# Kernel tuning notes

Measured on AMD Instinct MI355X. Metric: run time of the kernel, lower is better.

Reference implementation:

```python
import jax, jax.numpy as jnp
import numpy as np

EMBED = 1024

def setup_inputs() -> dict:
    key = jax.random.key(0)
    ks = jax.random.split(key, 7)
    s = 1.0 / np.sqrt(EMBED)  # ~ torch Linear default init scale
    x = jax.random.normal(ks[0], (4, 2048, EMBED), dtype=jnp.float32)
    Wq = jax.random.uniform(ks[1], (EMBED, EMBED), jnp.float32, -s, s)
    bq = jax.random.uniform(ks[2], (EMBED,), jnp.float32, -s, s)
    Wk = jax.random.uniform(ks[3], (EMBED, EMBED), jnp.float32, -s, s)
    bk = jax.random.uniform(ks[4], (EMBED,), jnp.float32, -s, s)
    Wv = jax.random.uniform(ks[5], (EMBED, EMBED), jnp.float32, -s, s)
    bv = jax.random.uniform(ks[6], (EMBED,), jnp.float32, -s, s)
    return {"x": x, "Wq": Wq, "bq": bq, "Wk": Wk, "bk": bk, "Wv": Wv, "bv": bv}

def reference(x, Wq, bq, Wk, bk, Wv, bv):
    # torch nn.Linear: y = x @ W.T + b
    q = jnp.einsum('bse,oe->bso', x, Wq) + bq
    k = jnp.einsum('bse,oe->bso', x, Wk) + bk
    v = jnp.einsum('bse,oe->bso', x, Wv) + bv
    scale = 1.0 / jnp.sqrt(jnp.float32(x.shape[-1]))
    scores = jnp.einsum('bqd,bkd->bqk', q, k) * scale  # [B,S,S]
    weights = jax.nn.softmax(scores, axis=-1)
    return jnp.einsum('bqk,bkd->bqd', weights, v)
```

## Files before the change

### kernel.cpp

```cpp
#include <hip/hip_runtime.h>
#include <stdint.h>

#define B_   4
#define S_   2048
#define E_   1024
#define MQKV (B_ * S_)
#define LDP  2112

typedef __bf16 bf16x8 __attribute__((ext_vector_type(8)));
typedef float f32x4 __attribute__((ext_vector_type(4)));
typedef unsigned short u16;
typedef unsigned int u32;

__device__ __forceinline__ u16 f2bf(float x) {
  union { float f; u32 u; } c; c.f = x;
  u32 r = (c.u + 0x7FFFu + ((c.u >> 16) & 1u)) >> 16;
  return (u16)r;
}
__device__ __forceinline__ float bf2f(u16 h) {
  union { u32 u; float f; } c; c.u = ((u32)h) << 16;
  return c.f;
}

__global__ __launch_bounds__(256) void cvt_f32_bf16(const float* __restrict__ src,
                                                    u16* __restrict__ dst, int n4) {
  int i = blockIdx.x * blockDim.x + threadIdx.x;
  int st = gridDim.x * blockDim.x;
  for (; i < n4; i += st) {
    float4 f = reinterpret_cast<const float4*>(src)[i];
    ushort4 o;
    o.x = f2bf(f.x); o.y = f2bf(f.y); o.z = f2bf(f.z); o.w = f2bf(f.w);
    reinterpret_cast<ushort4*>(dst)[i] = o;
  }
}

__global__ __launch_bounds__(256) void cvt_w3(const float* __restrict__ wq,
                                              const float* __restrict__ wk,
                                              const float* __restrict__ wv,
                                              u16* __restrict__ dst) {
  const int per = E_ * E_ / 4;
  int i = blockIdx.x * blockDim.x + threadIdx.x;
  const int sel = i / per;
  const int r = i - sel * per;
  const float* src = sel == 0 ? wq : (sel == 1 ? wk : wv);
  float4 f = reinterpret_cast<const float4*>(src)[r];
  ushort4 o;
  o.x = f2bf(f.x); o.y = f2bf(f.y); o.z = f2bf(f.z); o.w = f2bf(f.w);
  reinterpret_cast<ushort4*>(dst)[i] = o;
}

#define GLOAD_LDS16(g, l)                                                      \
  __builtin_amdgcn_global_load_lds(                                            \
      (const __attribute__((address_space(1))) u32*)(g),                       \
      (__attribute__((address_space(3))) u32*)(l), 16, 0, 0)

template <int BN, int EPI>
__global__ __launch_bounds__(512, 2) void gemm256(
    const u16* __restrict__ A, const u16* __restrict__ Bt, void* __restrict__ Cv,
    const float* __restrict__ b0, const float* __restrict__ b1,
    int N, int K, float scale,
    long sA, long sB, long sC, long ldA, long ldB, long ldC, int gx, int gy) {
  constexpr int BM = 256;
  constexpr int NR = BN / 64;
  constexpr int L  = 2 + BN / 128;
  constexpr int BSLOT = BN * 32;

  __shared__ alignas(16) u16 lds[4 * BM * 32 + 4 * BSLOT];
  u16* lA = lds;
  u16* lB = lds + 4 * BM * 32;

  const int t = threadIdx.x;
  const int wv = t >> 6;
  const int ln = t & 63;
  const int wm = wv >> 2;
  const int wn = wv & 3;

  const int nwg = gridDim.x;
  int id = blockIdx.x;
  id = (id & 7) * (nwg >> 3) + (id >> 3);
  const int pz = gx * gy;
  const int z = id / pz;
  const int r2 = id - z * pz;
  const int by = r2 / gx;
  const int bx = r2 - by * gx;
  const int bm = by * BM;
  const int bn = bx * BN;

  A += (size_t)z * sA;
  Bt += (size_t)z * sB;

  const int srow = t >> 2;
  const int g0 = (t & 3) ^ (srow & 3);
  const u16* gA0 = A + (size_t)(bm + srow) * ldA + g0 * 8;
  const u16* gA1 = gA0 + (size_t)128 * ldA;
  const u16* gB0 = Bt + (size_t)(bn + srow) * ldB + g0 * 8;
  const u16* gB1 = gB0 + (size_t)128 * ldB;

  auto STAGE = [&](int u) {
    const int s = u & 3;
    const int ko = u * 32;
    GLOAD_LDS16(gA0 + ko, lA + s * 8192 + wv * 512);
    GLOAD_LDS16(gA1 + ko, lA + s * 8192 + 4096 + wv * 512);
    GLOAD_LDS16(gB0 + ko, lB + s * BSLOT + wv * 512);
    if constexpr (BN == 256) GLOAD_LDS16(gB1 + ko, lB + s * BSLOT + 4096 + wv * 512);
  };

  const int lrow = ln & 15;
  const int g = ln >> 4;
  const int aR = wm * 128 + lrow;
  const int aOff = aR * 32 + (g ^ (aR & 3)) * 8;
  const int bR = wn * (BN / 4) + lrow;
  const int bOff = bR * 32 + (g ^ (bR & 3)) * 8;

  f32x4 acc[8][NR] = {};
  const int T = K >> 5;

  bf16x8 afA[8], afB[8], bgA[NR], bgB[NR];

#define RD_A(DST, TILE) do { const u16* _p = lA + ((TILE) & 3) * 8192 + aOff;  \
  _Pragma("unroll") for (int _i = 0; _i < 8; ++_i)                             \
    DST[_i] = *reinterpret_cast<const bf16x8*>(_p + _i * 512); } while (0)
#define RD_B(DST, TILE) do { const u16* _p = lB + ((TILE) & 3) * BSLOT + bOff; \
  _Pragma("unroll") for (int _j = 0; _j < NR; ++_j)                            \
    DST[_j] = *reinterpret_cast<const bf16x8*>(_p + _j * 512); } while (0)
#define DO_MFMA(AF, BG) do { __builtin_amdgcn_s_setprio(1);                    \
  _Pragma("unroll") for (int _i = 0; _i < 8; ++_i)                             \
  _Pragma("unroll") for (int _j = 0; _j < NR; ++_j)                            \
    acc[_i][_j] = __builtin_amdgcn_mfma_f32_16x16x32_bf16(AF[_i], BG[_j],      \
                                                          acc[_i][_j], 0, 0, 0);\
  __builtin_amdgcn_s_setprio(0); } while (0)
#define VM_GATE(COND) do {                                                     \
  if (COND) { asm volatile("s_waitcnt vmcnt(%0)" :: "n"(L) : "memory"); }      \
  else { asm volatile("s_waitcnt vmcnt(0)" ::: "memory"); }                    \
  __builtin_amdgcn_s_barrier(); asm volatile("" ::: "memory"); } while (0)

  STAGE(0); STAGE(1); STAGE(2);
  asm volatile("s_waitcnt vmcnt(%0)" :: "n"(L) : "memory");
  __builtin_amdgcn_s_barrier();
  asm volatile("" ::: "memory");

  if constexpr (NR == 2) { RD_A(afA, 0); RD_B(bgA, 0); }
  else                   { RD_B(bgA, 0); }

  for (int tt = 0; tt < T; tt += 2) {
    if (tt + 3 < T) STAGE(tt + 3);
    if constexpr (NR == 2) { RD_A(afB, tt + 1); RD_B(bgB, tt + 1); DO_MFMA(afA, bgA); }
    else                   { RD_A(afA, tt); RD_B(bgB, tt + 1);     DO_MFMA(afA, bgA); }
    VM_GATE(tt + 3 < T);

    if (tt + 4 < T) STAGE(tt + 4);
    if constexpr (NR == 2) {
      if (tt + 2 < T) { RD_A(afA, tt + 2); RD_B(bgA, tt + 2); }
      DO_MFMA(afB, bgB);
    } else {
      RD_A(afA, tt + 1);
      if (tt + 2 < T) RD_B(bgA, tt + 2);
      DO_MFMA(afA, bgB);
    }
    VM_GATE(tt + 4 < T);
  }
#undef RD_A
#undef RD_B
#undef DO_MFMA
#undef VM_GATE

  const int r0 = (ln >> 4) * 4;
  const int c0 = ln & 15;
#pragma unroll
  for (int i = 0; i < 8; ++i) {
#pragma unroll
    for (int j = 0; j < NR; ++j) {
      const int col = bn + wn * (BN / 4) + j * 16 + c0;
#pragma unroll
      for (int ii = 0; ii < 4; ++ii) {
        const int row = bm + wm * 128 + i * 16 + r0 + ii;
        float v = acc[i][j][ii];
        if constexpr (EPI == 0) {
          const int sel = col >> 10;
          const int cc = col & 1023;
          const float bb = sel == 0 ? b0[cc] : b1[cc];
          ((u16*)Cv)[(size_t)sel * 8388608 + (size_t)row * 1024 + cc] = f2bf(v + bb);
        } else if constexpr (EPI == 1) {
          ((u16*)Cv)[(size_t)z * sC + (size_t)row * ldC + col] = f2bf(v + b0[row]);
        } else if constexpr (EPI == 2) {
          ((u16*)Cv)[(size_t)z * sC + (size_t)row * ldC + col] = f2bf(__expf(v * scale));
        } else {
          ((float*)Cv)[(size_t)z * sC + (size_t)row * ldC + col] = v * b0[z * 2048 + row];
        }
      }
    }
  }
}

__global__ __launch_bounds__(256) void row_invsum(const u16* __restrict__ P,
                                                  float* __restrict__ invL) {
  const int row = blockIdx.x * 4 + (threadIdx.x >> 6);
  const int ln = threadIdx.x & 63;
  const u16* p = P + (size_t)row * LDP + ln * 32;
  float s = 0.f;
#pragma unroll
  for (int q = 0; q < 4; ++q) {
    uint4 r = reinterpret_cast<const uint4*>(p)[q];
    u32 w[4] = {r.x, r.y, r.z, r.w};
#pragma unroll
    for (int k = 0; k < 4; ++k) {
      s += bf2f((u16)(w[k] & 0xffffu));
      s += bf2f((u16)(w[k] >> 16));
    }
  }
  for (int o = 1; o < 64; o <<= 1) s += __shfl_xor(s, o);
  if (ln == 0) invL[row] = 1.0f / s;
}

extern "C" void kernel_launch(void* const* d_in, const int* in_sizes, int n_in,
                              void* d_out, int out_size, void* d_ws, size_t ws_size,
                              hipStream_t stream) {
  const float* x = (const float*)d_in[0];
  const float* Wq = (const float*)d_in[1];
  const float* bq = (const float*)d_in[2];
  const float* Wk = (const float*)d_in[3];
  const float* bk = (const float*)d_in[4];
  const float* Wv = (const float*)d_in[5];
  const float* bv = (const float*)d_in[6];
  float* out = (float*)d_out;

  const size_t xE = 8388608, wE = 3145728, qE = 8388608;
  const size_t vtE = (size_t)4 * 1024 * LDP;
  const size_t PmE = (size_t)4 * 2048 * LDP;
  const size_t need = (xE + wE + 2 * qE + vtE + PmE) * 2 + (size_t)MQKV * 4;
  if (ws_size < need) {
    hipMemsetAsync(d_out, 0, (size_t)out_size * sizeof(float), stream);
    return;
  }
  u16* xb = (u16*)d_ws;
  u16* wqkv = xb + xE;
  u16* qb = wqkv + wE;
  u16* vt = qb + 2 * qE;
  u16* Pm = vt + vtE;
  float* invL = (float*)(Pm + PmE);

  cvt_f32_bf16<<<2048, 256, 0, stream>>>(x, xb, MQKV * E_ / 4);
  cvt_w3<<<3 * E_ * E_ / 4 / 256, 256, 0, stream>>>(Wq, Wk, Wv, wqkv);

  gemm256<256, 0><<<256, 512, 0, stream>>>(
      xb, wqkv, qb, bq, bk, 2048, E_, 1.f,
      0, 0, 0, E_, E_, 1024, 8, 32);

  gemm256<128, 1><<<256, 512, 0, stream>>>(
      wqkv + 2 * (size_t)E_ * E_, xb, vt, bv, nullptr, 2048, E_, 1.f,
      0, (long)S_ * E_, (long)1024 * LDP, E_, E_, LDP, 16, 4);

  gemm256<256, 2><<<256, 512, 0, stream>>>(
      qb, qb + 8388608, Pm, nullptr, nullptr, 2048, E_, 0.03125f,
      (long)S_ * 1024, (long)S_ * 1024, (long)2048 * LDP, 1024, 1024, LDP, 8, 8);

  row_invsum<<<B_ * S_ / 4, 256, 0, stream>>>(Pm, invL);

  gemm256<128, 3><<<256, 512, 0, stream>>>(
      Pm, vt, out, invL, nullptr, E_, S_, 1.f,
      (long)2048 * LDP, (long)1024 * LDP, (long)S_ * E_, LDP, LDP, 1024, 8, 8);
}
```

Measured before the change: 166.7 us.

## Split-K the PV GEMM with atomic accumulation and change LDS swizzle

The final P·V GEMM moves from BN=128 tiles over the full K=2048 to BN=256 tiles with the K dimension split in two. Each half is handled by a separate set of workgroups that accumulate into a zeroed output with float atomics, and a memset of the output is added. The LDS XOR swizzle also changes from using row bits 0-1 to row bits 1-2 to reduce bank conflicts. The split keeps the grid at 256 workgroups while making tiles larger, at the cost of atomic traffic, an extra memset and a non-deterministic summation order.

```diff
diff --git a/kernel.cpp b/kernel.cpp
--- a/kernel.cpp
+++ b/kernel.cpp
@@ -54,7 +54,7 @@
       (const __attribute__((address_space(1))) u32*)(g),                       \
       (__attribute__((address_space(3))) u32*)(l), 16, 0, 0)
 
-template <int BN, int EPI>
+template <int BN, int EPI, int KS>
 __global__ __launch_bounds__(512, 2) void gemm256(
     const u16* __restrict__ A, const u16* __restrict__ Bt, void* __restrict__ Cv,
     const float* __restrict__ b0, const float* __restrict__ b1,
@@ -78,6 +78,12 @@
   const int nwg = gridDim.x;
   int id = blockIdx.x;
   id = (id & 7) * (nwg >> 3) + (id >> 3);
+  int ks = 0;
+  if constexpr (KS) {
+    const int half = nwg >> 1;
+    ks = id >= half;
+    id -= ks * half;
+  }
   const int pz = gx * gy;
   const int z = id / pz;
   const int r2 = id - z * pz;
@@ -86,11 +92,11 @@
   const int bm = by * BM;
   const int bn = bx * BN;
 
-  A += (size_t)z * sA;
-  Bt += (size_t)z * sB;
+  A += (size_t)z * sA + (size_t)ks * K;
+  Bt += (size_t)z * sB + (size_t)ks * K;
 
   const int srow = t >> 2;
-  const int g0 = (t & 3) ^ (srow & 3);
+  const int g0 = (t & 3) ^ ((srow >> 1) & 3);
   const u16* gA0 = A + (size_t)(bm + srow) * ldA + g0 * 8;
   const u16* gA1 = gA0 + (size_t)128 * ldA;
   const u16* gB0 = Bt + (size_t)(bn + srow) * ldB + g0 * 8;
@@ -108,9 +114,9 @@
   const int lrow = ln & 15;
   const int g = ln >> 4;
   const int aR = wm * 128 + lrow;
-  const int aOff = aR * 32 + (g ^ (aR & 3)) * 8;
+  const int aOff = aR * 32 + (g ^ ((aR >> 1) & 3)) * 8;
   const int bR = wn * (BN / 4) + lrow;
-  const int bOff = bR * 32 + (g ^ (bR & 3)) * 8;
+  const int bOff = bR * 32 + (g ^ ((bR >> 1) & 3)) * 8;
 
   f32x4 acc[8][NR] = {};
   const int T = K >> 5;
@@ -185,7 +191,9 @@
         } else if constexpr (EPI == 2) {
           ((u16*)Cv)[(size_t)z * sC + (size_t)row * ldC + col] = f2bf(__expf(v * scale));
         } else {
-          ((float*)Cv)[(size_t)z * sC + (size_t)row * ldC + col] = v * b0[z * 2048 + row];
+          const float sc = b0[z * 2048 + row];
+          unsafeAtomicAdd(&((float*)Cv)[(size_t)z * sC + (size_t)row * ldC + col],
+                          v * sc);
         }
       }
     }
@@ -242,21 +250,23 @@
   cvt_f32_bf16<<<2048, 256, 0, stream>>>(x, xb, MQKV * E_ / 4);
   cvt_w3<<<3 * E_ * E_ / 4 / 256, 256, 0, stream>>>(Wq, Wk, Wv, wqkv);
 
-  gemm256<256, 0><<<256, 512, 0, stream>>>(
+  hipMemsetAsync(out, 0, (size_t)MQKV * E_ * sizeof(float), stream);
+
+  gemm256<256, 0, 0><<<256, 512, 0, stream>>>(
       xb, wqkv, qb, bq, bk, 2048, E_, 1.f,
       0, 0, 0, E_, E_, 1024, 8, 32);
 
-  gemm256<128, 1><<<256, 512, 0, stream>>>(
+  gemm256<128, 1, 0><<<256, 512, 0, stream>>>(
       wqkv + 2 * (size_t)E_ * E_, xb, vt, bv, nullptr, 2048, E_, 1.f,
       0, (long)S_ * E_, (long)1024 * LDP, E_, E_, LDP, 16, 4);
 
-  gemm256<256, 2><<<256, 512, 0, stream>>>(
+  gemm256<256, 2, 0><<<256, 512, 0, stream>>>(
       qb, qb + 8388608, Pm, nullptr, nullptr, 2048, E_, 0.03125f,
       (long)S_ * 1024, (long)S_ * 1024, (long)2048 * LDP, 1024, 1024, LDP, 8, 8);
 
   row_invsum<<<B_ * S_ / 4, 256, 0, stream>>>(Pm, invL);
 
-  gemm256<128, 3><<<256, 512, 0, stream>>>(
-      Pm, vt, out, invL, nullptr, E_, S_, 1.f,
-      (long)2048 * LDP, (long)1024 * LDP, (long)S_ * E_, LDP, LDP, 1024, 8, 8);
-}
+  gemm256<256, 4, 1><<<256, 512, 0, stream>>>(
+      Pm, vt, out, invL, nullptr, E_, 1024, 1.f,
+      (long)2048 * LDP, (long)1024 * LDP, (long)S_ * E_, LDP, LDP, 1024, 4, 8);
+}
```

Result: slower. 200.6 us (+20.3%).

## Merge conversion kernels and QK/V projection launches, change LDS swizzle

Applied to the files above, without the earlier changes.

Folds the x and weight bf16 conversions into one grid-stride kernel, and runs the QK projection GEMM and the transposed V projection GEMM in a single 512-block launch that branches on block index. This removes launch gaps and lets the two projections share the GPU concurrently rather than each running on only 256 blocks. It also changes the LDS XOR swizzle to use (row>>1)&3, presumably to cut bank conflicts on the 16-byte fragment reads. The fused projection kernel now reserves the larger shared buffer for both branches, which could limit occupancy for the BN=128 path.

```diff
diff --git a/kernel.cpp b/kernel.cpp
--- a/kernel.cpp
+++ b/kernel.cpp
@@ -22,31 +22,28 @@
   return c.f;
 }
 
-__global__ __launch_bounds__(256) void cvt_f32_bf16(const float* __restrict__ src,
-                                                    u16* __restrict__ dst, int n4) {
-  int i = blockIdx.x * blockDim.x + threadIdx.x;
-  int st = gridDim.x * blockDim.x;
-  for (; i < n4; i += st) {
-    float4 f = reinterpret_cast<const float4*>(src)[i];
+__global__ __launch_bounds__(256) void cvt_all(
+    const float* __restrict__ x, const float* __restrict__ wq,
+    const float* __restrict__ wk, const float* __restrict__ wv,
+    u16* __restrict__ dst) {
+  const int gid = blockIdx.x * 256 + threadIdx.x;
+  const int total = 2097152 + 786432;
+  const int stride = gridDim.x * 256;
+  for (int i = gid; i < total; i += stride) {
+    float4 f;
+    if (i < 2097152) {
+      f = reinterpret_cast<const float4*>(x)[i];
+    } else {
+      const int j = i - 2097152;
+      const int sel = j >> 18;
+      const int r = j & 262143;
+      const float* s = sel == 0 ? wq : (sel == 1 ? wk : wv);
+      f = reinterpret_cast<const float4*>(s)[r];
+    }
     ushort4 o;
     o.x = f2bf(f.x); o.y = f2bf(f.y); o.z = f2bf(f.z); o.w = f2bf(f.w);
     reinterpret_cast<ushort4*>(dst)[i] = o;
   }
-}
-
-__global__ __launch_bounds__(256) void cvt_w3(const float* __restrict__ wq,
-                                              const float* __restrict__ wk,
-                                              const float* __restrict__ wv,
-                                              u16* __restrict__ dst) {
-  const int per = E_ * E_ / 4;
-  int i = blockIdx.x * blockDim.x + threadIdx.x;
-  const int sel = i / per;
-  const int r = i - sel * per;
-  const float* src = sel == 0 ? wq : (sel == 1 ? wk : wv);
-  float4 f = reinterpret_cast<const float4*>(src)[r];
-  ushort4 o;
-  o.x = f2bf(f.x); o.y = f2bf(f.y); o.z = f2bf(f.z); o.w = f2bf(f.w);
-  reinterpret_cast<ushort4*>(dst)[i] = o;
 }
 
 #define GLOAD_LDS16(g, l)                                                      \
@@ -55,7 +52,8 @@
       (__attribute__((address_space(3))) u32*)(l), 16, 0, 0)
 
 template <int BN, int EPI>
-__global__ __launch_bounds__(512, 2) void gemm256(
+__device__ __forceinline__ void gemm_body(
+    u16* __restrict__ ldsb, int id, int nwg,
     const u16* __restrict__ A, const u16* __restrict__ Bt, void* __restrict__ Cv,
     const float* __restrict__ b0, const float* __restrict__ b1,
     int N, int K, float scale,
@@ -65,9 +63,8 @@
   constexpr int L  = 2 + BN / 128;
   constexpr int BSLOT = BN * 32;
 
-  __shared__ alignas(16) u16 lds[4 * BM * 32 + 4 * BSLOT];
-  u16* lA = lds;
-  u16* lB = lds + 4 * BM * 32;
+  u16* lA = ldsb;
+  u16* lB = ldsb + 4 * BM * 32;
 
   const int t = threadIdx.x;
   const int wv = t >> 6;
@@ -75,8 +72,6 @@
   const int wm = wv >> 2;
   const int wn = wv & 3;
 
-  const int nwg = gridDim.x;
-  int id = blockIdx.x;
   id = (id & 7) * (nwg >> 3) + (id >> 3);
   const int pz = gx * gy;
   const int z = id / pz;
@@ -90,7 +85,7 @@
   Bt += (size_t)z * sB;
 
   const int srow = t >> 2;
-  const int g0 = (t & 3) ^ (srow & 3);
+  const int g0 = (t & 3) ^ ((srow >> 1) & 3);
   const u16* gA0 = A + (size_t)(bm + srow) * ldA + g0 * 8;
   const u16* gA1 = gA0 + (size_t)128 * ldA;
   const u16* gB0 = Bt + (size_t)(bn + srow) * ldB + g0 * 8;
@@ -108,9 +103,9 @@
   const int lrow = ln & 15;
   const int g = ln >> 4;
   const int aR = wm * 128 + lrow;
-  const int aOff = aR * 32 + (g ^ (aR & 3)) * 8;
+  const int aOff = aR * 32 + (g ^ ((aR >> 1) & 3)) * 8;
   const int bR = wn * (BN / 4) + lrow;
-  const int bOff = bR * 32 + (g ^ (bR & 3)) * 8;
+  const int bOff = bR * 32 + (g ^ ((bR >> 1) & 3)) * 8;
 
   f32x4 acc[8][NR] = {};
   const int T = K >> 5;
@@ -192,6 +187,43 @@
   }
 }
 
+__global__ __launch_bounds__(512, 2) void proj_k(
+    const u16* __restrict__ xb, const u16* __restrict__ wqkv,
+    u16* __restrict__ qb, u16* __restrict__ vt,
+    const float* __restrict__ bq, const float* __restrict__ bk,
+    const float* __restrict__ bv) {
+  __shared__ alignas(16) u16 lds[65536];
+  if (blockIdx.x < 256) {
+    gemm_body<256, 0>(lds, blockIdx.x, 256,
+                      xb, wqkv, qb, bq, bk, 2048, E_, 1.f,
+                      0, 0, 0, E_, E_, 1024, 8, 32);
+  } else {
+    gemm_body<128, 1>(lds, blockIdx.x - 256, 256,
+                      wqkv + 2 * (size_t)E_ * E_, xb, vt, bv, nullptr,
+                      2048, E_, 1.f,
+                      0, (long)S_ * E_, (long)1024 * LDP, E_, E_, LDP, 16, 4);
+  }
+}
+
+__global__ __launch_bounds__(512, 2) void qkt_k(
+    const u16* __restrict__ qb, u16* __restrict__ Pm) {
+  __shared__ alignas(16) u16 lds[65536];
+  gemm_body<256, 2>(lds, blockIdx.x, 256,
+                    qb, qb + 8388608, Pm, nullptr, nullptr, 2048, E_, 0.03125f,
+                    (long)S_ * 1024, (long)S_ * 1024, (long)2048 * LDP,
+                    1024, 1024, LDP, 8, 8);
+}
+
+__global__ __launch_bounds__(512, 2) void pv_k(
+    const u16* __restrict__ Pm, const u16* __restrict__ vt,
+    float* __restrict__ out, const float* __restrict__ invL) {
+  __shared__ alignas(16) u16 lds[49152];
+  gemm_body<128, 3>(lds, blockIdx.x, 256,
+                    Pm, vt, out, invL, nullptr, E_, S_, 1.f,
+                    (long)2048 * LDP, (long)1024 * LDP, (long)S_ * E_,
+                    LDP, LDP, 1024, 8, 8);
+}
+
 __global__ __launch_bounds__(256) void row_invsum(const u16* __restrict__ P,
                                                   float* __restrict__ invL) {
   const int row = blockIdx.x * 4 + (threadIdx.x >> 6);
@@ -239,24 +271,13 @@
   u16* Pm = vt + vtE;
   float* invL = (float*)(Pm + PmE);
 
-  cvt_f32_bf16<<<2048, 256, 0, stream>>>(x, xb, MQKV * E_ / 4);
-  cvt_w3<<<3 * E_ * E_ / 4 / 256, 256, 0, stream>>>(Wq, Wk, Wv, wqkv);
-
-  gemm256<256, 0><<<256, 512, 0, stream>>>(
-      xb, wqkv, qb, bq, bk, 2048, E_, 1.f,
-      0, 0, 0, E_, E_, 1024, 8, 32);
-
-  gemm256<128, 1><<<256, 512, 0, stream>>>(
-      wqkv + 2 * (size_t)E_ * E_, xb, vt, bv, nullptr, 2048, E_, 1.f,
-      0, (long)S_ * E_, (long)1024 * LDP, E_, E_, LDP, 16, 4);
-
-  gemm256<256, 2><<<256, 512, 0, stream>>>(
-      qb, qb + 8388608, Pm, nullptr, nullptr, 2048, E_, 0.03125f,
-      (long)S_ * 1024, (long)S_ * 1024, (long)2048 * LDP, 1024, 1024, LDP, 8, 8);
+  cvt_all<<<2048, 256, 0, stream>>>(x, Wq, Wk, Wv, xb);
+
+  proj_k<<<512, 512, 0, stream>>>(xb, wqkv, qb, vt, bq, bk, bv);
+
+  qkt_k<<<256, 512, 0, stream>>>(qb, Pm);
 
   row_invsum<<<B_ * S_ / 4, 256, 0, stream>>>(Pm, invL);
 
-  gemm256<128, 3><<<256, 512, 0, stream>>>(
-      Pm, vt, out, invL, nullptr, E_, S_, 1.f,
-      (long)2048 * LDP, (long)1024 * LDP, (long)S_ * E_, LDP, LDP, 1024, 8, 8);
-}
+  pv_k<<<256, 512, 0, stream>>>(Pm, vt, out, invL);
+}
```

Measured after the change: 150.1 us. 9.9% less time.
